# Kernel optimization log

Hardware: AMD Instinct MI355X
Metric: run time of the kernel (lower is better)

## Reference

```python
import jax, jax.numpy as jnp
import numpy as np

HEADS = 16
LN_EPS = 1e-5

def setup_inputs() -> dict:
    key = jax.random.key(0)
    ks = jax.random.split(key, 8)
    B, S, NT = 4, 1024, 1024
    sc = 1.0 / np.sqrt(NT)
    return {
        "x": jax.random.normal(ks[0], (B, S, NT), dtype=jnp.float32),
        "Wq": jax.random.normal(ks[1], (NT, NT), dtype=jnp.float32) * sc,
        "bq": jax.random.normal(ks[2], (NT,), dtype=jnp.float32) * 0.02,
        "Wk": jax.random.normal(ks[3], (NT, NT), dtype=jnp.float32) * sc,
        "bk": jax.random.normal(ks[4], (NT,), dtype=jnp.float32) * 0.02,
        "Wv": jax.random.normal(ks[5], (NT, NT), dtype=jnp.float32) * sc,
        "bv": jax.random.normal(ks[6], (NT,), dtype=jnp.float32) * 0.02,
        "gamma": jnp.ones((NT,), dtype=jnp.float32),
        "beta": jnp.zeros((NT,), dtype=jnp.float32),
    }

def reference(x, Wq, bq, Wk, bk, Wv, bv, gamma, beta):
    B, S, nt = x.shape
    heads = HEADS
    dph = nt // heads
    # torch nn.Linear: y = x @ W.T + b
    q = x @ Wq.T + bq
    k = x @ Wk.T + bk
    v = x @ Wv.T + bv
    # torch .view(B*heads, -1, dph) is a row-major reshape (interleaved split)
    q = q.reshape(B * heads, -1, dph)
    k = k.reshape(B * heads, -1, dph)
    v = v.reshape(B * heads, -1, dph)
    # scaled scores; scale uses last dim of the score matrix (== seq len here)
    att = jnp.einsum('bid,bjd->bij', q, k)
    scale = att.shape[-1] ** (-0.5)
    att = jax.nn.softmax(jax.nn.relu(att * scale), axis=-1)
    # dropout in eval mode -> identity
    at_sum_sum = att.sum(axis=1).reshape(B, heads, -1)  # [B, heads, S]
    context = jnp.einsum('bij,bjd->bid', att, v).reshape(B, -1, nt)
    h = x + context
    mu = h.mean(axis=-1, keepdims=True)
    var = h.var(axis=-1, keepdims=True)
    out = (h - mu) * jax.lax.rsqrt(var + LN_EPS) * gamma + beta
    return out, at_sum_sum
```

## Files before the change

### kernel.cpp

```cpp
#include <hip/hip_runtime.h>
#include <hip/hip_bf16.h>
#include <cstdint>
#include <cstddef>


typedef short short8 __attribute__((ext_vector_type(8)));
typedef short short4v __attribute__((ext_vector_type(4)));
typedef float f32x4 __attribute__((ext_vector_type(4)));

#define MFMA32(a, b, c) __builtin_amdgcn_mfma_f32_16x16x32_bf16(a, b, c, 0, 0, 0)
#define MFMA16x16(a, b, c) __builtin_amdgcn_mfma_f32_16x16x16bf16_1k(a, b, c, 0, 0, 0)
#define ATT_SCALE 0.03125f

__device__ __forceinline__ short f2bf(float f) {
  union { float f; uint32_t u; } x; x.f = f;
  uint32_t u = x.u + 0x7fffu + ((x.u >> 16) & 1u);
  return (short)(u >> 16);
}

__device__ __forceinline__ uint32_t pk_bf16_trunc(float lo, float hi) {
  return __builtin_amdgcn_perm(__float_as_uint(hi), __float_as_uint(lo),
                               0x07060302u);
}

#define GLDS16(gp, lp)                                                        \
  __builtin_amdgcn_global_load_lds(                                           \
      (const __attribute__((address_space(1))) void*)(gp),                    \
      (__attribute__((address_space(3))) void*)(lp), 16, 0, 0)
#define GLDS4(gp, lp)                                                         \
  __builtin_amdgcn_global_load_lds(                                           \
      (const __attribute__((address_space(1))) void*)(gp),                    \
      (__attribute__((address_space(3))) void*)(lp), 4, 0, 0)

__global__ __launch_bounds__(256) void convert_kernel(
    const float* __restrict__ x, const float* __restrict__ wq,
    const float* __restrict__ wk, const float* __restrict__ wv,
    short* __restrict__ xb, short* __restrict__ wb) {
  const long XN = 4L * 1024 * 1024, WN = 1024L * 1024;
  long e = (long)(blockIdx.x * blockDim.x + threadIdx.x) * 4;
  const float* src; short* dst;
  if (e < XN)               { src = x  + e;                dst = xb + e; }
  else if (e < XN + WN)     { src = wq + (e - XN);         dst = wb + (e - XN); }
  else if (e < XN + 2 * WN) { src = wk + (e - XN - WN);    dst = wb + (e - XN); }
  else                      { src = wv + (e - XN - 2*WN);  dst = wb + (e - XN); }
  f32x4 v = *(const f32x4*)src;
  short4v o;
  o[0] = f2bf(v[0]); o[1] = f2bf(v[1]); o[2] = f2bf(v[2]); o[3] = f2bf(v[3]);
  *(short4v*)dst = o;
}

__global__ __launch_bounds__(256, 3) void qkv_gemm(
    const short* __restrict__ xb, const short* __restrict__ wb,
    const float* __restrict__ bq, const float* __restrict__ bk,
    const float* __restrict__ bv, short* __restrict__ qb,
    short* __restrict__ kb, short* __restrict__ vtp) {
  __shared__ short As[128 * 32];
  __shared__ short Bs[128 * 32];
  const int tid = threadIdx.x;
  const int lane = tid & 63;
  const int lm = lane & 15, quad = lane >> 4;
  const int wave = tid >> 6, wy = wave >> 1, wx = wave & 1;
  const int m0 = blockIdx.y * 128, n0 = blockIdx.x * 128;
  const int z = blockIdx.z;
  const short* w = wb + (size_t)z * (1024 * 1024);
  const float* bias = (z == 0) ? bq : (z == 1) ? bk : bv;
  const float scl = (z == 0) ? ATT_SCALE : 1.0f;

  const short* gA0 = xb + (size_t)(m0 + (tid >> 2)) * 1024 + (tid & 3) * 8;
  const short* gA1 = gA0 + 64 * 1024;
  const short* gB0 = w  + (size_t)(n0 + (tid >> 2)) * 1024 + (tid & 3) * 8;
  const short* gB1 = gB0 + 64 * 1024;
  short* lA0 = As + tid * 8;
  short* lA1 = As + (tid + 256) * 8;
  short* lB0 = Bs + tid * 8;
  short* lB1 = Bs + (tid + 256) * 8;

  f32x4 acc[4][4];
#pragma unroll
  for (int i = 0; i < 4; i++)
#pragma unroll
    for (int j = 0; j < 4; j++) acc[i][j] = (f32x4){0.f, 0.f, 0.f, 0.f};

  for (int k0 = 0; k0 < 1024; k0 += 32) {
    GLDS16(gA0 + k0, lA0);
    GLDS16(gA1 + k0, lA1);
    GLDS16(gB0 + k0, lB0);
    GLDS16(gB1 + k0, lB1);
    __syncthreads();
    short8 a[4], b[4];
#pragma unroll
    for (int t = 0; t < 4; t++)
      a[t] = *(const short8*)(As + (wy * 64 + t * 16 + lm) * 32 + quad * 8);
#pragma unroll
    for (int t = 0; t < 4; t++)
      b[t] = *(const short8*)(Bs + (wx * 64 + t * 16 + lm) * 32 + quad * 8);
#pragma unroll
    for (int mt = 0; mt < 4; mt++)
#pragma unroll
      for (int nt = 0; nt < 4; nt++)
        acc[mt][nt] = MFMA32(a[mt], b[nt], acc[mt][nt]);
    __syncthreads();
  }
  if (z == 2) {
#pragma unroll
    for (int nt = 0; nt < 4; nt++) {
      const int n = n0 + wx * 64 + nt * 16 + lm;
      const float bn = bias[n];
      const size_t nbase = (size_t)((n >> 4) & 3) * 16384 +
                           (size_t)((((n >> 8) & 3) * 16 + (n & 15)) * 4 +
                                    ((n >> 6) & 3));
#pragma unroll
      for (int mt = 0; mt < 4; mt++) {
#pragma unroll
        for (int r = 0; r < 4; r++) {
          const int m = m0 + wy * 64 + mt * 16 + quad * 4 + r;
          vtp[(size_t)(m >> 6) * 65536 + nbase + (size_t)(m & 63) * 256] =
              f2bf(acc[mt][nt][r] + bn);
        }
      }
    }
  } else {
    short* out = (z == 0) ? qb : kb;
#pragma unroll
    for (int nt = 0; nt < 4; nt++) {
      const int n = n0 + wx * 64 + nt * 16 + lm;
      const float bn = bias[n];
#pragma unroll
      for (int mt = 0; mt < 4; mt++) {
        const int mb = m0 + wy * 64 + mt * 16 + quad * 4;
#pragma unroll
        for (int r = 0; r < 4; r++)
          out[(size_t)(mb + r) * 1024 + n] = f2bf((acc[mt][nt][r] + bn) * scl);
      }
    }
  }
}

__global__ __launch_bounds__(256, 4) void attn_kernel(
    const short* __restrict__ qb, const short* __restrict__ kb,
    const short* __restrict__ vtp, const float* __restrict__ x,
    const float* __restrict__ gamma, const float* __restrict__ beta,
    float* __restrict__ out1, float* __restrict__ rvW) {
  __shared__ short Ks[2][64 * 64];
  __shared__ short Vs[2][4 * 4 * 256];

  const int tid = threadIdx.x;
  const int lane = tid & 63, wave = tid >> 6;
  const int lm = lane & 15, quad = lane >> 4;
  const int h = blockIdx.x >> 4, bb = blockIdx.x & 15;
  const short* Qh = qb + (size_t)h * 65536;
  const short* Kh = kb + (size_t)h * 65536;
  const short* Vp = vtp + (size_t)h * 65536;
  const int i0 = bb * 64 + wave * 16;

  const short8 qA0 = *(const short8*)(Qh + (size_t)(i0 + lm) * 64 + quad * 8);
  const short8 qA1 = *(const short8*)(Qh + (size_t)(i0 + lm) * 64 + 32 + quad * 8);

  const int c0 = tid, c1 = tid + 256;
  const short* gK0 = Kh + (size_t)(c0 >> 3) * 64 + ((c0 & 7) ^ ((c0 >> 3) & 7)) * 8;
  const short* gK1 = Kh + (size_t)(c1 >> 3) * 64 + ((c1 & 7) ^ ((c1 >> 3) & 7)) * 8;
  const short* gV0 = Vp + (c0 >> 7) * 16384 + ((c0 >> 5) & 3) * 256 + (c0 & 31) * 8;
  const short* gV1 = Vp + (c1 >> 7) * 16384 + ((c1 >> 5) & 3) * 256 + (c1 & 31) * 8;
  const int lK0 = c0 * 8, lK1 = c1 * 8;

  f32x4 acc[4];
#pragma unroll
  for (int t = 0; t < 4; t++) acc[t] = (f32x4){0.f, 0.f, 0.f, 0.f};
  float ds[4] = {0.f, 0.f, 0.f, 0.f};

  const int swz0 = (quad ^ (lm & 7)) * 8;
  const int swz1 = ((quad + 4) ^ (lm & 7)) * 8;

  GLDS16(gK0, &Ks[0][0] + lK0);
  GLDS16(gK1, &Ks[0][0] + lK1);
  GLDS16(gV0, &Vs[0][0] + lK0);
  GLDS16(gV1, &Vs[0][0] + lK1);

  for (int ch = 0; ch < 16; ch++) {
    const int b = ch & 1;
    __syncthreads();
    if (ch < 15) {
      const int ko = (ch + 1) * 4096, vo = (ch + 1) * 1024;
      GLDS16(gK0 + ko, &Ks[b ^ 1][0] + lK0);
      GLDS16(gK1 + ko, &Ks[b ^ 1][0] + lK1);
      GLDS16(gV0 + vo, &Vs[b ^ 1][0] + lK0);
      GLDS16(gV1 + vo, &Vs[b ^ 1][0] + lK1);
    }
#pragma unroll
    for (int jj = 0; jj < 4; jj++) {
      const short* krow = &Ks[b][(jj * 16 + lm) * 64];
      const short8 kf0 = *(const short8*)(krow + swz0);
      const short8 kf1 = *(const short8*)(krow + swz1);
      f32x4 z = {0.f, 0.f, 0.f, 0.f};
      z = MFMA32(kf0, qA0, z);
      z = MFMA32(kf1, qA1, z);
      float p[4];
#pragma unroll
      for (int r = 0; r < 4; r++) {
        p[r] = __expf(fmaxf(z[r], 0.f));
        ds[r] += p[r];
      }
      union { uint32_t u[2]; short4v s; } pu;
      pu.u[0] = pk_bf16_trunc(p[0], p[1]);
      pu.u[1] = pk_bf16_trunc(p[2], p[3]);
      const short* vbase = &Vs[b][jj * 256 + lane * 4];
#pragma unroll
      for (int dt = 0; dt < 4; dt++) {
        const short4v vtf = *(const short4v*)(vbase + dt * 1024);
        acc[dt] = MFMA16x16(vtf, pu.s, acc[dt]);
      }
    }
  }
  float t = (ds[0] + ds[1]) + (ds[2] + ds[3]);
  t += __shfl_xor(t, 16);
  t += __shfl_xor(t, 32);
  const float rv = 1.f / t;
  if (lane < 16) rvW[h * 1024 + i0 + lm] = rv;

  const int m = h * 64 + bb * 4 + wave;
  const int nb = lm * 64 + quad * 4;
  const float* xr = x + (size_t)m * 1024;
  float hv[4][4], s1 = 0.f, s2 = 0.f;
#pragma unroll
  for (int dt = 0; dt < 4; dt++) {
    f32x4 xv = *(const f32x4*)(xr + nb + dt * 16);
#pragma unroll
    for (int r = 0; r < 4; r++) {
      const float v = xv[r] + acc[dt][r] * rv;
      hv[dt][r] = v; s1 += v; s2 += v * v;
    }
  }
#pragma unroll
  for (int mk = 1; mk < 64; mk <<= 1) {
    s1 += __shfl_xor(s1, mk);
    s2 += __shfl_xor(s2, mk);
  }
  const float mu = s1 * (1.f / 1024.f);
  const float var = s2 * (1.f / 1024.f) - mu * mu;
  const float rstd = rsqrtf(var + 1e-5f);
  float* orow = out1 + (size_t)m * 1024;
#pragma unroll
  for (int dt = 0; dt < 4; dt++) {
    f32x4 gv = *(const f32x4*)(gamma + nb + dt * 16);
    f32x4 bv2 = *(const f32x4*)(beta + nb + dt * 16);
    f32x4 ov;
#pragma unroll
    for (int r = 0; r < 4; r++)
      ov[r] = (hv[dt][r] - mu) * rstd * gv[r] + bv2[r];
    *(f32x4*)(orow + nb + dt * 16) = ov;
  }
}

__global__ __launch_bounds__(256, 4) void colsum_kernel(
    const short* __restrict__ qb, const short* __restrict__ kb,
    const float* __restrict__ rvW, float* __restrict__ out2) {
  __shared__ short Qs[2][64 * 64];
  __shared__ float rvS[2][64];

  const int tid = threadIdx.x;
  const int lane = tid & 63, wave = tid >> 6;
  const int lm = lane & 15, quad = lane >> 4;
  const int h = blockIdx.x >> 4, jb = blockIdx.x & 15;
  const int j0 = jb * 64 + wave * 16;
  const short* Qh = qb + (size_t)h * 65536;
  const short* Kh = kb + (size_t)h * 65536;
  const float* rvh = rvW + h * 1024;

  const short* krr = Kh + (size_t)(j0 + lm) * 64 + quad * 8;
  const short8 kf0 = *(const short8*)krr;
  const short8 kf1 = *(const short8*)(krr + 32);

  const int c0 = tid, c1 = tid + 256;
  const short* gQ0 = Qh + (size_t)(c0 >> 3) * 64 + ((c0 & 7) ^ ((c0 >> 3) & 7)) * 8;
  const short* gQ1 = Qh + (size_t)(c1 >> 3) * 64 + ((c1 & 7) ^ ((c1 >> 3) & 7)) * 8;
  const int lQ0 = c0 * 8, lQ1 = c1 * 8;

  const int swz0 = (quad ^ (lm & 7)) * 8;
  const int swz1 = ((quad + 4) ^ (lm & 7)) * 8;

  f32x4 cs = {0.f, 0.f, 0.f, 0.f};

  GLDS16(gQ0, &Qs[0][0] + lQ0);
  GLDS16(gQ1, &Qs[0][0] + lQ1);
  if (wave == 0) GLDS4(rvh + lane, &rvS[0][0]);

  for (int ch = 0; ch < 16; ch++) {
    const int b = ch & 1;
    __syncthreads();
    if (ch < 15) {
      const int qo = (ch + 1) * 4096;
      GLDS16(gQ0 + qo, &Qs[b ^ 1][0] + lQ0);
      GLDS16(gQ1 + qo, &Qs[b ^ 1][0] + lQ1);
      if (wave == 0) GLDS4(rvh + (ch + 1) * 64 + lane, &rvS[b ^ 1][0]);
    }
#pragma unroll
    for (int ii = 0; ii < 4; ii++) {
      const short* qrow = &Qs[b][(ii * 16 + lm) * 64];
      const short8 qf0 = *(const short8*)(qrow + swz0);
      const short8 qf1 = *(const short8*)(qrow + swz1);
      f32x4 z = {0.f, 0.f, 0.f, 0.f};
      z = MFMA32(kf0, qf0, z);
      z = MFMA32(kf1, qf1, z);
      const float rvv = rvS[b][ii * 16 + lm];
#pragma unroll
      for (int r = 0; r < 4; r++)
        cs[r] += __expf(fmaxf(z[r], 0.f)) * rvv;
    }
  }
#pragma unroll
  for (int mk = 1; mk < 16; mk <<= 1)
#pragma unroll
    for (int r = 0; r < 4; r++) cs[r] += __shfl_xor(cs[r], mk);
  if (lm == 0)
    *(f32x4*)(out2 + h * 1024 + j0 + quad * 4) = cs;
}

extern "C" void kernel_launch(void* const* d_in, const int* in_sizes, int n_in,
                              void* d_out, int out_size, void* d_ws, size_t ws_size,
                              hipStream_t stream) {
  const float* x  = (const float*)d_in[0];
  const float* Wq = (const float*)d_in[1];
  const float* bq = (const float*)d_in[2];
  const float* Wk = (const float*)d_in[3];
  const float* bk = (const float*)d_in[4];
  const float* Wv = (const float*)d_in[5];
  const float* bv = (const float*)d_in[6];
  const float* gamma = (const float*)d_in[7];
  const float* beta  = (const float*)d_in[8];

  float* out1 = (float*)d_out;
  float* out2 = out1 + 4L * 1024 * 1024;

  short* xb = (short*)d_ws;
  short* wb = xb + 4L * 1024 * 1024;
  short* qb = wb + 3L * 1024 * 1024;
  short* kb = qb + 4L * 1024 * 1024;
  short* vtp = kb + 4L * 1024 * 1024;
  float* rvW = (float*)wb;

  convert_kernel<<<7168, 256, 0, stream>>>(x, Wq, Wk, Wv, xb, wb);
  qkv_gemm<<<dim3(8, 32, 3), 256, 0, stream>>>(xb, wb, bq, bk, bv, qb, kb, vtp);
  attn_kernel<<<1024, 256, 0, stream>>>(qb, kb, vtp, x, gamma, beta, out1, rvW);
  colsum_kernel<<<1024, 256, 0, stream>>>(qb, kb, rvW, out2);
}
```

Measured before the change: 183.5 us.

## Process two 16-row tiles per wave in attention and colsum kernels

Each wave now handles two 16-row query tiles (attention) or two key tiles (colsum) instead of one. Every K/V or Q fragment read from shared memory feeds twice as many MFMAs, and the per-block global load traffic is amortized over 128 rows. The grids shrink from 1024 to 512 blocks and the launch bounds drop to 2 blocks per CU to make room for the doubled accumulators. The cost is fewer waves in flight, so less latency hiding, and only 512 blocks for 256 CUs.

New measurement: 182.7 us. About the same (-0.4%).

```diff
diff --git a/kernel.cpp b/kernel.cpp
--- a/kernel.cpp
+++ b/kernel.cpp
@@ -136,7 +136,7 @@
   }
 }
 
-__global__ __launch_bounds__(256, 4) void attn_kernel(
+__global__ __launch_bounds__(256, 2) void attn_kernel(
     const short* __restrict__ qb, const short* __restrict__ kb,
     const short* __restrict__ vtp, const float* __restrict__ x,
     const float* __restrict__ gamma, const float* __restrict__ beta,
@@ -147,14 +147,16 @@
   const int tid = threadIdx.x;
   const int lane = tid & 63, wave = tid >> 6;
   const int lm = lane & 15, quad = lane >> 4;
-  const int h = blockIdx.x >> 4, bb = blockIdx.x & 15;
+  const int h = blockIdx.x >> 3, bb = blockIdx.x & 7;
   const short* Qh = qb + (size_t)h * 65536;
   const short* Kh = kb + (size_t)h * 65536;
   const short* Vp = vtp + (size_t)h * 65536;
-  const int i0 = bb * 64 + wave * 16;
+  const int i0 = bb * 128 + wave * 32;
 
   const short8 qA0 = *(const short8*)(Qh + (size_t)(i0 + lm) * 64 + quad * 8);
   const short8 qA1 = *(const short8*)(Qh + (size_t)(i0 + lm) * 64 + 32 + quad * 8);
+  const short8 qB0 = *(const short8*)(Qh + (size_t)(i0 + 16 + lm) * 64 + quad * 8);
+  const short8 qB1 = *(const short8*)(Qh + (size_t)(i0 + 16 + lm) * 64 + 32 + quad * 8);
 
   const int c0 = tid, c1 = tid + 256;
   const short* gK0 = Kh + (size_t)(c0 >> 3) * 64 + ((c0 & 7) ^ ((c0 >> 3) & 7)) * 8;
@@ -163,10 +165,14 @@
   const short* gV1 = Vp + (c1 >> 7) * 16384 + ((c1 >> 5) & 3) * 256 + (c1 & 31) * 8;
   const int lK0 = c0 * 8, lK1 = c1 * 8;
 
-  f32x4 acc[4];
-#pragma unroll
-  for (int t = 0; t < 4; t++) acc[t] = (f32x4){0.f, 0.f, 0.f, 0.f};
-  float ds[4] = {0.f, 0.f, 0.f, 0.f};
+  f32x4 accA[4], accB[4];
+#pragma unroll
+  for (int t = 0; t < 4; t++) {
+    accA[t] = (f32x4){0.f, 0.f, 0.f, 0.f};
+    accB[t] = (f32x4){0.f, 0.f, 0.f, 0.f};
+  }
+  float dsA[4] = {0.f, 0.f, 0.f, 0.f};
+  float dsB[4] = {0.f, 0.f, 0.f, 0.f};
 
   const int swz0 = (quad ^ (lm & 7)) * 8;
   const int swz1 = ((quad + 4) ^ (lm & 7)) * 8;
@@ -191,67 +197,88 @@
       const short* krow = &Ks[b][(jj * 16 + lm) * 64];
       const short8 kf0 = *(const short8*)(krow + swz0);
       const short8 kf1 = *(const short8*)(krow + swz1);
-      f32x4 z = {0.f, 0.f, 0.f, 0.f};
-      z = MFMA32(kf0, qA0, z);
-      z = MFMA32(kf1, qA1, z);
-      float p[4];
+      f32x4 zA = {0.f, 0.f, 0.f, 0.f};
+      zA = MFMA32(kf0, qA0, zA);
+      zA = MFMA32(kf1, qA1, zA);
+      f32x4 zB = {0.f, 0.f, 0.f, 0.f};
+      zB = MFMA32(kf0, qB0, zB);
+      zB = MFMA32(kf1, qB1, zB);
+      float pA[4], pB[4];
 #pragma unroll
       for (int r = 0; r < 4; r++) {
-        p[r] = __expf(fmaxf(z[r], 0.f));
-        ds[r] += p[r];
-      }
-      union { uint32_t u[2]; short4v s; } pu;
-      pu.u[0] = pk_bf16_trunc(p[0], p[1]);
-      pu.u[1] = pk_bf16_trunc(p[2], p[3]);
+        pA[r] = __expf(fmaxf(zA[r], 0.f));
+        dsA[r] += pA[r];
+        pB[r] = __expf(fmaxf(zB[r], 0.f));
+        dsB[r] += pB[r];
+      }
+      union { uint32_t u[2]; short4v s; } puA, puB;
+      puA.u[0] = pk_bf16_trunc(pA[0], pA[1]);
+      puA.u[1] = pk_bf16_trunc(pA[2], pA[3]);
+      puB.u[0] = pk_bf16_trunc(pB[0], pB[1]);
+      puB.u[1] = pk_bf16_trunc(pB[2], pB[3]);
       const short* vbase = &Vs[b][jj * 256 + lane * 4];
 #pragma unroll
       for (int dt = 0; dt < 4; dt++) {
         const short4v vtf = *(const short4v*)(vbase + dt * 1024);
-        acc[dt] = MFMA16x16(vtf, pu.s, acc[dt]);
-      }
-    }
-  }
-  float t = (ds[0] + ds[1]) + (ds[2] + ds[3]);
-  t += __shfl_xor(t, 16);
-  t += __shfl_xor(t, 32);
-  const float rv = 1.f / t;
-  if (lane < 16) rvW[h * 1024 + i0 + lm] = rv;
-
-  const int m = h * 64 + bb * 4 + wave;
+        accA[dt] = MFMA16x16(vtf, puA.s, accA[dt]);
+        accB[dt] = MFMA16x16(vtf, puB.s, accB[dt]);
+      }
+    }
+  }
+  float tA = (dsA[0] + dsA[1]) + (dsA[2] + dsA[3]);
+  tA += __shfl_xor(tA, 16);
+  tA += __shfl_xor(tA, 32);
+  float tB = (dsB[0] + dsB[1]) + (dsB[2] + dsB[3]);
+  tB += __shfl_xor(tB, 16);
+  tB += __shfl_xor(tB, 32);
+  const float rvA = 1.f / tA;
+  const float rvB = 1.f / tB;
+  if (lane < 16) {
+    rvW[h * 1024 + i0 + lm] = rvA;
+    rvW[h * 1024 + i0 + 16 + lm] = rvB;
+  }
+
+  const int mA = h * 64 + bb * 8 + wave * 2;
   const int nb = lm * 64 + quad * 4;
-  const float* xr = x + (size_t)m * 1024;
-  float hv[4][4], s1 = 0.f, s2 = 0.f;
-#pragma unroll
-  for (int dt = 0; dt < 4; dt++) {
-    f32x4 xv = *(const f32x4*)(xr + nb + dt * 16);
-#pragma unroll
-    for (int r = 0; r < 4; r++) {
-      const float v = xv[r] + acc[dt][r] * rv;
-      hv[dt][r] = v; s1 += v; s2 += v * v;
-    }
-  }
-#pragma unroll
-  for (int mk = 1; mk < 64; mk <<= 1) {
-    s1 += __shfl_xor(s1, mk);
-    s2 += __shfl_xor(s2, mk);
-  }
-  const float mu = s1 * (1.f / 1024.f);
-  const float var = s2 * (1.f / 1024.f) - mu * mu;
-  const float rstd = rsqrtf(var + 1e-5f);
-  float* orow = out1 + (size_t)m * 1024;
-#pragma unroll
-  for (int dt = 0; dt < 4; dt++) {
-    f32x4 gv = *(const f32x4*)(gamma + nb + dt * 16);
-    f32x4 bv2 = *(const f32x4*)(beta + nb + dt * 16);
-    f32x4 ov;
-#pragma unroll
-    for (int r = 0; r < 4; r++)
-      ov[r] = (hv[dt][r] - mu) * rstd * gv[r] + bv2[r];
-    *(f32x4*)(orow + nb + dt * 16) = ov;
-  }
-}
-
-__global__ __launch_bounds__(256, 4) void colsum_kernel(
+#pragma unroll
+  for (int tile = 0; tile < 2; tile++) {
+    const int m = mA + tile;
+    const f32x4* accT = tile ? accB : accA;
+    const float rv = tile ? rvB : rvA;
+    const float* xr = x + (size_t)m * 1024;
+    float hv[4][4], s1 = 0.f, s2 = 0.f;
+#pragma unroll
+    for (int dt = 0; dt < 4; dt++) {
+      f32x4 xv = *(const f32x4*)(xr + nb + dt * 16);
+#pragma unroll
+      for (int r = 0; r < 4; r++) {
+        const float v = xv[r] + accT[dt][r] * rv;
+        hv[dt][r] = v; s1 += v; s2 += v * v;
+      }
+    }
+#pragma unroll
+    for (int mk = 1; mk < 64; mk <<= 1) {
+      s1 += __shfl_xor(s1, mk);
+      s2 += __shfl_xor(s2, mk);
+    }
+    const float mu = s1 * (1.f / 1024.f);
+    const float var = s2 * (1.f / 1024.f) - mu * mu;
+    const float rstd = rsqrtf(var + 1e-5f);
+    float* orow = out1 + (size_t)m * 1024;
+#pragma unroll
+    for (int dt = 0; dt < 4; dt++) {
+      f32x4 gv = *(const f32x4*)(gamma + nb + dt * 16);
+      f32x4 bv2 = *(const f32x4*)(beta + nb + dt * 16);
+      f32x4 ov;
+#pragma unroll
+      for (int r = 0; r < 4; r++)
+        ov[r] = (hv[dt][r] - mu) * rstd * gv[r] + bv2[r];
+      *(f32x4*)(orow + nb + dt * 16) = ov;
+    }
+  }
+}
+
+__global__ __launch_bounds__(256, 2) void colsum_kernel(
     const short* __restrict__ qb, const short* __restrict__ kb,
     const float* __restrict__ rvW, float* __restrict__ out2) {
   __shared__ short Qs[2][64 * 64];
@@ -260,15 +287,18 @@
   const int tid = threadIdx.x;
   const int lane = tid & 63, wave = tid >> 6;
   const int lm = lane & 15, quad = lane >> 4;
-  const int h = blockIdx.x >> 4, jb = blockIdx.x & 15;
-  const int j0 = jb * 64 + wave * 16;
+  const int h = blockIdx.x >> 3, jb = blockIdx.x & 7;
+  const int j0 = jb * 128 + wave * 32;
   const short* Qh = qb + (size_t)h * 65536;
   const short* Kh = kb + (size_t)h * 65536;
   const float* rvh = rvW + h * 1024;
 
-  const short* krr = Kh + (size_t)(j0 + lm) * 64 + quad * 8;
-  const short8 kf0 = *(const short8*)krr;
-  const short8 kf1 = *(const short8*)(krr + 32);
+  const short* krA = Kh + (size_t)(j0 + lm) * 64 + quad * 8;
+  const short8 kA0 = *(const short8*)krA;
+  const short8 kA1 = *(const short8*)(krA + 32);
+  const short* krB = Kh + (size_t)(j0 + 16 + lm) * 64 + quad * 8;
+  const short8 kB0 = *(const short8*)krB;
+  const short8 kB1 = *(const short8*)(krB + 32);
 
   const int c0 = tid, c1 = tid + 256;
   const short* gQ0 = Qh + (size_t)(c0 >> 3) * 64 + ((c0 & 7) ^ ((c0 >> 3) & 7)) * 8;
@@ -278,7 +308,8 @@
   const int swz0 = (quad ^ (lm & 7)) * 8;
   const int swz1 = ((quad + 4) ^ (lm & 7)) * 8;
 
-  f32x4 cs = {0.f, 0.f, 0.f, 0.f};
+  f32x4 csA = {0.f, 0.f, 0.f, 0.f};
+  f32x4 csB = {0.f, 0.f, 0.f, 0.f};
 
   GLDS16(gQ0, &Qs[0][0] + lQ0);
   GLDS16(gQ1, &Qs[0][0] + lQ1);
@@ -298,21 +329,31 @@
       const short* qrow = &Qs[b][(ii * 16 + lm) * 64];
       const short8 qf0 = *(const short8*)(qrow + swz0);
       const short8 qf1 = *(const short8*)(qrow + swz1);
-      f32x4 z = {0.f, 0.f, 0.f, 0.f};
-      z = MFMA32(kf0, qf0, z);
-      z = MFMA32(kf1, qf1, z);
+      f32x4 zA = {0.f, 0.f, 0.f, 0.f};
+      zA = MFMA32(kA0, qf0, zA);
+      zA = MFMA32(kA1, qf1, zA);
+      f32x4 zB = {0.f, 0.f, 0.f, 0.f};
+      zB = MFMA32(kB0, qf0, zB);
+      zB = MFMA32(kB1, qf1, zB);
       const float rvv = rvS[b][ii * 16 + lm];
 #pragma unroll
-      for (int r = 0; r < 4; r++)
-        cs[r] += __expf(fmaxf(z[r], 0.f)) * rvv;
+      for (int r = 0; r < 4; r++) {
+        csA[r] += __expf(fmaxf(zA[r], 0.f)) * rvv;
+        csB[r] += __expf(fmaxf(zB[r], 0.f)) * rvv;
+      }
     }
   }
 #pragma unroll
   for (int mk = 1; mk < 16; mk <<= 1)
 #pragma unroll
-    for (int r = 0; r < 4; r++) cs[r] += __shfl_xor(cs[r], mk);
-  if (lm == 0)
-    *(f32x4*)(out2 + h * 1024 + j0 + quad * 4) = cs;
+    for (int r = 0; r < 4; r++) {
+      csA[r] += __shfl_xor(csA[r], mk);
+      csB[r] += __shfl_xor(csB[r], mk);
+    }
+  if (lm == 0) {
+    *(f32x4*)(out2 + h * 1024 + j0 + quad * 4) = csA;
+    *(f32x4*)(out2 + h * 1024 + j0 + 16 + quad * 4) = csB;
+  }
 }
 
 extern "C" void kernel_launch(void* const* d_in, const int* in_sizes, int n_in,
@@ -340,6 +381,6 @@
 
   convert_kernel<<<7168, 256, 0, stream>>>(x, Wq, Wk, Wv, xb, wb);
   qkv_gemm<<<dim3(8, 32, 3), 256, 0, stream>>>(xb, wb, bq, bk, bv, qb, kb, vtp);
-  attn_kernel<<<1024, 256, 0, stream>>>(qb, kb, vtp, x, gamma, beta, out1, rvW);
-  colsum_kernel<<<1024, 256, 0, stream>>>(qb, kb, rvW, out2);
-}
+  attn_kernel<<<512, 256, 0, stream>>>(qb, kb, vtp, x, gamma, beta, out1, rvW);
+  colsum_kernel<<<512, 256, 0, stream>>>(qb, kb, rvW, out2);
+}
```
